# Kernel tuning notes

Hardware: AMD Instinct MI355X
Metric: run time of the kernel (lower is better)

## Reference

```python
import jax, jax.numpy as jnp
import numpy as np

E, TOPK, H, I = 8, 2, 2048, 5632
T = 4096


def setup_inputs() -> dict:
    key = jax.random.key(0)
    k1, k2, k3, k4 = jax.random.split(key, 4)
    hidden_states = jax.random.normal(k1, (T, H), dtype=jnp.float32)
    gate_w = jax.random.normal(k2, (E, H), dtype=jnp.float32) * (1.0 / np.sqrt(H))
    # fused gate+up projection: [E, 2*I, H]
    w13 = jax.random.normal(k3, (E, 2 * I, H), dtype=jnp.float32) * (1.0 / np.sqrt(H))
    # down projection: [E, H, I]
    w2 = jax.random.normal(k4, (E, H, I), dtype=jnp.float32) * (1.0 / np.sqrt(I))
    return {"hidden_states": hidden_states, "gate_w": gate_w, "w13": w13, "w2": w2, "top_k": TOPK}


def reference(hidden_states, gate_w, w13, w2, top_k):
    num_experts = gate_w.shape[0]
    inter = w2.shape[2]
    # router: fp32 gate logits -> softmax -> top-k -> renormalize (FusedMoE renormalize=True)
    logits = hidden_states.astype(jnp.float32) @ gate_w.T          # [T, E]
    probs = jax.nn.softmax(logits, axis=-1)
    vals, idx = jax.lax.top_k(probs, top_k)                        # [T, k]
    vals = vals / jnp.sum(vals, axis=-1, keepdims=True)
    # dense routing weight matrix [T, E] (zero outside top-k)
    dense_w = jnp.sum(jax.nn.one_hot(idx, num_experts, dtype=vals.dtype) * vals[..., None], axis=1)

    def body(acc, inputs):
        w13_e, w2_e, we = inputs                                   # [2I,H], [H,I], [T]
        gu = hidden_states @ w13_e.T                               # [T, 2I]
        g, u = gu[:, :inter], gu[:, inter:]
        h = jax.nn.silu(g) * u                                     # SwiGLU
        y = h @ w2_e.T                                             # [T, H]
        return acc + we[:, None] * y, None

    acc0 = jnp.zeros_like(hidden_states)
    out, _ = jax.lax.scan(body, acc0, (w13, w2, dense_w.T))
    return out
```

## Files before the change

### kernel.cpp

```cpp
#include <hip/hip_runtime.h>

#define T_TOK 4096
#define H_DIM 2048
#define I_DIM 5632
#define NE 8

typedef _Float16 f16;
typedef _Float16 f16x8 __attribute__((ext_vector_type(8)));
typedef _Float16 f16x4 __attribute__((ext_vector_type(4)));
typedef float f32x4 __attribute__((ext_vector_type(4)));

#define OFF_META   0
#define OFF_BTOK   256
#define OFF_BW     (256 + 32768)
#define OFF_RE     (256 + 2 * 32768)
#define OFF_RW     (256 + 3 * 32768)
#define OFF_HSB    (256 + 4 * 32768)
#define OFF_HB     (OFF_HSB + (size_t)T_TOK * H_DIM * 2)

__device__ __forceinline__ int swzk(int r, int bir) {
    return (bir & 15) | ((((bir >> 4) ^ r) & 7) << 4);
}

__device__ __forceinline__ f16x4 cvt4(float4 v) {
    f16x4 t; t[0] = (f16)v.x; t[1] = (f16)v.y; t[2] = (f16)v.z; t[3] = (f16)v.w; return t;
}

__global__ void cvt_hs_kernel(const float* __restrict__ hs, f16* __restrict__ hsb) {
    size_t i = ((size_t)blockIdx.x * 256 + threadIdx.x) * 8;
    float4 a = *(const float4*)(hs + i);
    float4 b = *(const float4*)(hs + i + 4);
    f16x8 v;
    v[0] = (f16)a.x; v[1] = (f16)a.y; v[2] = (f16)a.z; v[3] = (f16)a.w;
    v[4] = (f16)b.x; v[5] = (f16)b.y; v[6] = (f16)b.z; v[7] = (f16)b.w;
    *(f16x8*)(hsb + i) = v;
}

__global__ void gate_kernel(const float* __restrict__ hs, const float* __restrict__ gw,
                            int* __restrict__ re, float* __restrict__ rw,
                            int* __restrict__ counts) {
    int lane = threadIdx.x & 63;
    int t = blockIdx.x * 4 + (threadIdx.x >> 6);
    float acc[NE];
#pragma unroll
    for (int e = 0; e < NE; ++e) acc[e] = 0.f;
    const float* x = hs + (size_t)t * H_DIM;
    for (int i = lane; i < H_DIM; i += 64) {
        float xv = x[i];
#pragma unroll
        for (int e = 0; e < NE; ++e) acc[e] += xv * gw[e * H_DIM + i];
    }
#pragma unroll
    for (int e = 0; e < NE; ++e)
        for (int off = 32; off > 0; off >>= 1) acc[e] += __shfl_xor(acc[e], off);
    if (lane == 0) {
        int i1 = 0; float l1 = acc[0];
#pragma unroll
        for (int e = 1; e < NE; ++e) if (acc[e] > l1) { l1 = acc[e]; i1 = e; }
        int i2 = -1; float l2 = -1e30f;
#pragma unroll
        for (int e = 0; e < NE; ++e) if (e != i1 && acc[e] > l2) { l2 = acc[e]; i2 = e; }
        float aa = __expf(l2 - l1);
        float s = 1.f / (1.f + aa);
        re[t * 2] = i1; re[t * 2 + 1] = i2;
        rw[t * 2] = s;  rw[t * 2 + 1] = aa * s;
        atomicAdd(&counts[i1], 1);
        atomicAdd(&counts[i2], 1);
    }
}

__global__ void scan_kernel(int* __restrict__ meta) {
    if (threadIdx.x == 0) {
        int s = 0;
        for (int e = 0; e < NE; ++e) { meta[8 + e] = s; meta[16 + e] = s; s += meta[e]; }
    }
}

__global__ void place_kernel(const int* __restrict__ re, const float* __restrict__ rw,
                             int* __restrict__ cursor, int* __restrict__ btok,
                             float* __restrict__ bwv) {
    int t = blockIdx.x * 256 + threadIdx.x;
    if (t >= T_TOK) return;
#pragma unroll
    for (int s = 0; s < 2; ++s) {
        int e = re[t * 2 + s];
        int p = atomicAdd(&cursor[e], 1);
        btok[p] = t;
        bwv[p] = rw[t * 2 + s];
    }
}

__device__ __forceinline__ void decode_panel(int id, int npx, int e_arg,
                                             int& e, int& bx, int& by) {
    int sg  = id >> 8;
    int rem = id & 255;
    by = rem >> 3;
    int P = sg * 8 + (rem & 7);
    if (e_arg >= 0) { e = e_arg; bx = P; }
    else            { e = P / npx; bx = P % npx; }
}

__global__ __launch_bounds__(512) void gemm1_kernel(
    const float* __restrict__ w13, const f16* __restrict__ hsb, f16* __restrict__ hb,
    const int* __restrict__ counts, const int* __restrict__ offs,
    const int* __restrict__ btok, int e_arg, int global_h)
{
    int e, bx, by;
    decode_panel(blockIdx.x, 88, e_arg, e, bx, by);
    const int n_e = counts[e];
    if (by * 128 >= n_e) return;
    const int boff = offs[e];
    const float* We = w13 + (size_t)e * (2 * I_DIM) * H_DIM;

    const int tid = threadIdx.x;
    const int lane = tid & 63;
    const int wid = tid >> 6;
    const int wm = wid >> 1, wn = wid & 1;

    __shared__ f16 As0[128 * 64], As1[128 * 64];
    __shared__ f16 Bg0[64 * 64],  Bg1[64 * 64];
    __shared__ f16 Bu0[64 * 64],  Bu1[64 * 64];

    const f16* gA[2];
    int awadr[2];
#pragma unroll
    for (int i = 0; i < 2; ++i) {
        int c = i * 512 + tid;
        int r = c >> 3;
        int s = c & 7;
        int idx = by * 128 + r;
        idx = idx < n_e ? idx : n_e - 1;
        int tok = btok[boff + idx];
        gA[i] = hsb + (size_t)tok * H_DIM + s * 8;
        awadr[i] = r * 128 + swzk(r, s * 16);
    }
    const float* gBg[2]; const float* gBu[2];
    int bwadr[2];
#pragma unroll
    for (int j = 0; j < 2; ++j) {
        int c = j * 512 + tid;
        int r = c >> 4;
        int k4 = c & 15;
        gBg[j] = We + (size_t)(bx * 64 + r) * H_DIM + k4 * 4;
        gBu[j] = We + (size_t)(I_DIM + bx * 64 + r) * H_DIM + k4 * 4;
        bwadr[j] = r * 128 + swzk(r, k4 * 8);
    }

    f32x4 accg[2][2], accu[2][2];
#pragma unroll
    for (int m = 0; m < 2; ++m)
#pragma unroll
        for (int n = 0; n < 2; ++n) { accg[m][n] = (f32x4)0.f; accu[m][n] = (f32x4)0.f; }

    const int NT = H_DIM / 64;

    {
        f16x8 aP[2]; float4 gP[2], uP[2];
#pragma unroll
        for (int i = 0; i < 2; ++i) aP[i] = *(const f16x8*)(gA[i]);
#pragma unroll
        for (int j = 0; j < 2; ++j) { gP[j] = *(const float4*)gBg[j]; uP[j] = *(const float4*)gBu[j]; }
#pragma unroll
        for (int i = 0; i < 2; ++i) *(f16x8*)((char*)As0 + awadr[i]) = aP[i];
#pragma unroll
        for (int j = 0; j < 2; ++j) {
            *(f16x4*)((char*)Bg0 + bwadr[j]) = cvt4(gP[j]);
            *(f16x4*)((char*)Bu0 + bwadr[j]) = cvt4(uP[j]);
        }
        __syncthreads();
    }

#define G1_TILE(AsR, BgR, BuR, AsW, BgW, BuW, t)                                    \
    {                                                                               \
        const int kn = (((t) + 1 < NT) ? (t) + 1 : NT - 1) * 64;                    \
        f16x8 aN[2]; float4 gN[2], uN[2];                                           \
        _Pragma("unroll")                                                           \
        for (int i = 0; i < 2; ++i) aN[i] = *(const f16x8*)(gA[i] + kn);            \
        _Pragma("unroll")                                                           \
        for (int j = 0; j < 2; ++j) {                                               \
            gN[j] = *(const float4*)(gBg[j] + kn);                                  \
            uN[j] = *(const float4*)(gBu[j] + kn);                                  \
        }                                                                           \
        _Pragma("unroll")                                                           \
        for (int kh = 0; kh < 2; ++kh) {                                            \
            f16x8 a[2], bg[2], bu[2];                                               \
            const int kb = kh * 64 + (lane >> 4) * 16;                              \
            _Pragma("unroll")                                                       \
            for (int m = 0; m < 2; ++m) {                                           \
                int r = wm * 32 + m * 16 + (lane & 15);                             \
                a[m] = *(const f16x8*)((const char*)AsR + r * 128 + swzk(r, kb));   \
            }                                                                       \
            _Pragma("unroll")                                                       \
            for (int n = 0; n < 2; ++n) {                                           \
                int r = wn * 32 + n * 16 + (lane & 15);                             \
                bg[n] = *(const f16x8*)((const char*)BgR + r * 128 + swzk(r, kb));  \
                bu[n] = *(const f16x8*)((const char*)BuR + r * 128 + swzk(r, kb));  \
            }                                                                       \
            _Pragma("unroll")                                                       \
            for (int m = 0; m < 2; ++m)                                             \
                _Pragma("unroll")                                                   \
                for (int n = 0; n < 2; ++n) {                                       \
                    accg[m][n] = __builtin_amdgcn_mfma_f32_16x16x32_f16(a[m], bg[n], accg[m][n], 0, 0, 0); \
                    accu[m][n] = __builtin_amdgcn_mfma_f32_16x16x32_f16(a[m], bu[n], accu[m][n], 0, 0, 0); \
                }                                                                   \
        }                                                                           \
        _Pragma("unroll")                                                           \
        for (int i = 0; i < 2; ++i) *(f16x8*)((char*)AsW + awadr[i]) = aN[i];       \
        _Pragma("unroll")                                                           \
        for (int j = 0; j < 2; ++j) {                                               \
            *(f16x4*)((char*)BgW + bwadr[j]) = cvt4(gN[j]);                         \
            *(f16x4*)((char*)BuW + bwadr[j]) = cvt4(uN[j]);                         \
        }                                                                           \
        __syncthreads();                                                            \
    }

#pragma unroll 1
    for (int kt = 0; kt < NT; kt += 2) {
        G1_TILE(As0, Bg0, Bu0, As1, Bg1, Bu1, kt);
        G1_TILE(As1, Bg1, Bu1, As0, Bg0, Bu0, kt + 1);
    }
#undef G1_TILE

    const int hbase = (global_h ? boff : 0) + by * 128;
#pragma unroll
    for (int m = 0; m < 2; ++m) {
        int rl0 = wm * 32 + m * 16 + ((lane >> 4) << 2);
#pragma unroll
        for (int r = 0; r < 4; ++r) {
            int rl = rl0 + r;
            if (by * 128 + rl < n_e) {
#pragma unroll
                for (int n = 0; n < 2; ++n) {
                    float g = accg[m][n][r];
                    float u = accu[m][n][r];
                    float h = g / (1.f + __expf(-g)) * u;
                    hb[(size_t)(hbase + rl) * I_DIM + bx * 64 + wn * 32 + n * 16 + (lane & 15)] = (f16)h;
                }
            }
        }
    }
}

__global__ __launch_bounds__(512) void gemm2_kernel(
    const float* __restrict__ w2, const f16* __restrict__ hb, float* __restrict__ out,
    const int* __restrict__ counts, const int* __restrict__ offs,
    const int* __restrict__ btok, const float* __restrict__ bwv, int e_arg, int global_h)
{
    int e, bx, by;
    decode_panel(blockIdx.x, 16, e_arg, e, bx, by);
    const int n_e = counts[e];
    if (by * 128 >= n_e) return;
    const int boff = offs[e];
    const float* We = w2 + (size_t)e * H_DIM * I_DIM;

    const int tid = threadIdx.x;
    const int lane = tid & 63;
    const int wid = tid >> 6;
    const int wm = wid >> 1, wn = wid & 1;

    __shared__ f16 As0[128 * 64], As1[128 * 64];
    __shared__ f16 Bs0[128 * 64], Bs1[128 * 64];

    const int hbase = (global_h ? boff : 0) + by * 128;
    const f16* gA[2];
    int awadr[2];
#pragma unroll
    for (int i = 0; i < 2; ++i) {
        int c = i * 512 + tid;
        int r = c >> 3;
        int s = c & 7;
        gA[i] = hb + (size_t)(hbase + r) * I_DIM + s * 8;
        awadr[i] = r * 128 + swzk(r, s * 16);
    }
    const float* gB[4];
    int bwadr[4];
#pragma unroll
    for (int j = 0; j < 4; ++j) {
        int c = j * 512 + tid;
        int r = c >> 4;
        int k4 = c & 15;
        gB[j] = We + (size_t)(bx * 128 + r) * I_DIM + k4 * 4;
        bwadr[j] = r * 128 + swzk(r, k4 * 8);
    }

    f32x4 acc[2][4];
#pragma unroll
    for (int m = 0; m < 2; ++m)
#pragma unroll
        for (int n = 0; n < 4; ++n) acc[m][n] = (f32x4)0.f;

    const int NT = I_DIM / 64;

    {
        f16x8 aP[2]; float4 bP[4];
#pragma unroll
        for (int i = 0; i < 2; ++i) aP[i] = *(const f16x8*)(gA[i]);
#pragma unroll
        for (int j = 0; j < 4; ++j) bP[j] = *(const float4*)gB[j];
#pragma unroll
        for (int i = 0; i < 2; ++i) *(f16x8*)((char*)As0 + awadr[i]) = aP[i];
#pragma unroll
        for (int j = 0; j < 4; ++j) *(f16x4*)((char*)Bs0 + bwadr[j]) = cvt4(bP[j]);
        __syncthreads();
    }

#define G2_TILE(AsR, BsR, AsW, BsW, t)                                              \
    {                                                                               \
        const int kn = (((t) + 1 < NT) ? (t) + 1 : NT - 1) * 64;                    \
        f16x8 aN[2]; float4 bN[4];                                                  \
        _Pragma("unroll")                                                           \
        for (int i = 0; i < 2; ++i) aN[i] = *(const f16x8*)(gA[i] + kn);            \
        _Pragma("unroll")                                                           \
        for (int j = 0; j < 4; ++j) bN[j] = *(const float4*)(gB[j] + kn);           \
        _Pragma("unroll")                                                           \
        for (int kh = 0; kh < 2; ++kh) {                                            \
            f16x8 a[2], b[4];                                                       \
            const int kb = kh * 64 + (lane >> 4) * 16;                              \
            _Pragma("unroll")                                                       \
            for (int m = 0; m < 2; ++m) {                                           \
                int r = wm * 32 + m * 16 + (lane & 15);                             \
                a[m] = *(const f16x8*)((const char*)AsR + r * 128 + swzk(r, kb));   \
            }                                                                       \
            _Pragma("unroll")                                                       \
            for (int n = 0; n < 4; ++n) {                                           \
                int r = wn * 64 + n * 16 + (lane & 15);                             \
                b[n] = *(const f16x8*)((const char*)BsR + r * 128 + swzk(r, kb));   \
            }                                                                       \
            _Pragma("unroll")                                                       \
            for (int m = 0; m < 2; ++m)                                             \
                _Pragma("unroll")                                                   \
                for (int n = 0; n < 4; ++n)                                         \
                    acc[m][n] = __builtin_amdgcn_mfma_f32_16x16x32_f16(a[m], b[n], acc[m][n], 0, 0, 0); \
        }                                                                           \
        _Pragma("unroll")                                                           \
        for (int i = 0; i < 2; ++i) *(f16x8*)((char*)AsW + awadr[i]) = aN[i];       \
        _Pragma("unroll")                                                           \
        for (int j = 0; j < 4; ++j) *(f16x4*)((char*)BsW + bwadr[j]) = cvt4(bN[j]); \
        __syncthreads();                                                            \
    }

#pragma unroll 1
    for (int kt = 0; kt < NT; kt += 2) {
        G2_TILE(As0, Bs0, As1, Bs1, kt);
        G2_TILE(As1, Bs1, As0, Bs0, kt + 1);
    }
#undef G2_TILE

#pragma unroll
    for (int m = 0; m < 2; ++m) {
        int rl0 = wm * 32 + m * 16 + ((lane >> 4) << 2);
#pragma unroll
        for (int r = 0; r < 4; ++r) {
            int rl = rl0 + r;
            if (by * 128 + rl < n_e) {
                int p = boff + by * 128 + rl;
                int tok = btok[p];
                float w = bwv[p];
#pragma unroll
                for (int n = 0; n < 4; ++n)
                    atomicAdd(&out[(size_t)tok * H_DIM + bx * 128 + wn * 64 + n * 16 + (lane & 15)],
                              w * acc[m][n][r]);
            }
        }
    }
}

extern "C" void kernel_launch(void* const* d_in, const int* in_sizes, int n_in,
                              void* d_out, int out_size, void* d_ws, size_t ws_size,
                              hipStream_t stream) {
    const float* hs  = (const float*)d_in[0];
    const float* gw  = (const float*)d_in[1];
    const float* w13 = (const float*)d_in[2];
    const float* w2  = (const float*)d_in[3];
    float* out = (float*)d_out;

    char* ws = (char*)d_ws;
    int*   meta = (int*)(ws + OFF_META);
    int*   btok = (int*)(ws + OFF_BTOK);
    float* bwv  = (float*)(ws + OFF_BW);
    int*   re   = (int*)(ws + OFF_RE);
    float* rw   = (float*)(ws + OFF_RW);
    f16*   hsb  = (f16*)(ws + OFF_HSB);
    f16*   hb   = (f16*)(ws + OFF_HB);

    hipMemsetAsync(d_out, 0, (size_t)T_TOK * H_DIM * 4, stream);
    hipMemsetAsync(meta, 0, 256, stream);

    cvt_hs_kernel<<<(T_TOK * H_DIM) / (256 * 8), 256, 0, stream>>>(hs, hsb);
    gate_kernel<<<T_TOK / 4, 256, 0, stream>>>(hs, gw, re, rw, meta);
    scan_kernel<<<1, 64, 0, stream>>>(meta);
    place_kernel<<<T_TOK / 256, 256, 0, stream>>>(re, rw, meta + 16, btok, bwv);

    size_t need_allpairs = OFF_HB + (size_t)(2 * T_TOK + 128) * I_DIM * 2;
    if (ws_size >= need_allpairs) {
        gemm1_kernel<<<704 * 32, 512, 0, stream>>>(w13, hsb, hb, meta, meta + 8, btok, -1, 1);
        gemm2_kernel<<<128 * 32, 512, 0, stream>>>(w2, hb, out, meta, meta + 8, btok, bwv, -1, 1);
    } else {
        for (int e = 0; e < NE; ++e) {
            gemm1_kernel<<<88 * 32, 512, 0, stream>>>(w13, hsb, hb, meta, meta + 8, btok, e, 0);
            gemm2_kernel<<<16 * 32, 512, 0, stream>>>(w2, hb, out, meta, meta + 8, btok, bwv, e, 0);
        }
    }
}
```

Measured before the change: 1.330 ms.

## Pre-convert weights to fp16 and stream tiles via direct global-to-LDS loads

```diff
diff --git a/kernel.cpp b/kernel.cpp
--- a/kernel.cpp
+++ b/kernel.cpp
@@ -7,7 +7,6 @@
 
 typedef _Float16 f16;
 typedef _Float16 f16x8 __attribute__((ext_vector_type(8)));
-typedef _Float16 f16x4 __attribute__((ext_vector_type(4)));
 typedef float f32x4 __attribute__((ext_vector_type(4)));
 
 #define OFF_META   0
@@ -16,14 +15,26 @@
 #define OFF_RE     (256 + 2 * 32768)
 #define OFF_RW     (256 + 3 * 32768)
 #define OFF_HSB    (256 + 4 * 32768)
-#define OFF_HB     (OFF_HSB + (size_t)T_TOK * H_DIM * 2)
+#define OFF_WF     (OFF_HSB + (size_t)T_TOK * H_DIM * 2)
+
+typedef const __attribute__((address_space(1))) unsigned int guint;
+typedef __attribute__((address_space(3))) unsigned int luint;
 
 __device__ __forceinline__ int swzk(int r, int bir) {
     return (bir & 15) | ((((bir >> 4) ^ r) & 7) << 4);
 }
 
-__device__ __forceinline__ f16x4 cvt4(float4 v) {
-    f16x4 t; t[0] = (f16)v.x; t[1] = (f16)v.y; t[2] = (f16)v.z; t[3] = (f16)v.w; return t;
+__global__ void cvt_w_kernel(const float* __restrict__ src, f16* __restrict__ dst, int n8) {
+    int stride = gridDim.x * blockDim.x;
+    for (int i = blockIdx.x * blockDim.x + threadIdx.x; i < n8; i += stride) {
+        size_t b = (size_t)i * 8;
+        float4 a = *(const float4*)(src + b);
+        float4 c = *(const float4*)(src + b + 4);
+        f16x8 v;
+        v[0] = (f16)a.x; v[1] = (f16)a.y; v[2] = (f16)a.z; v[3] = (f16)a.w;
+        v[4] = (f16)c.x; v[5] = (f16)c.y; v[6] = (f16)c.z; v[7] = (f16)c.w;
+        *(f16x8*)(dst + b) = v;
+    }
 }
 
 __global__ void cvt_hs_kernel(const float* __restrict__ hs, f16* __restrict__ hsb) {
@@ -92,16 +103,16 @@
 
 __device__ __forceinline__ void decode_panel(int id, int npx, int e_arg,
                                              int& e, int& bx, int& by) {
+    if (e_arg >= 0) { e = e_arg; bx = id >> 5; by = id & 31; return; }
     int sg  = id >> 8;
     int rem = id & 255;
     by = rem >> 3;
     int P = sg * 8 + (rem & 7);
-    if (e_arg >= 0) { e = e_arg; bx = P; }
-    else            { e = P / npx; bx = P % npx; }
-}
-
-__global__ __launch_bounds__(512) void gemm1_kernel(
-    const float* __restrict__ w13, const f16* __restrict__ hsb, f16* __restrict__ hb,
+    e = P / npx; bx = P % npx;
+}
+
+__global__ __launch_bounds__(256, 2) void gemm1_kernel(
+    const f16* __restrict__ w13f, const f16* __restrict__ hsb, f16* __restrict__ hb,
     const int* __restrict__ counts, const int* __restrict__ offs,
     const int* __restrict__ btok, int e_arg, int global_h)
 {
@@ -110,139 +121,113 @@
     const int n_e = counts[e];
     if (by * 128 >= n_e) return;
     const int boff = offs[e];
-    const float* We = w13 + (size_t)e * (2 * I_DIM) * H_DIM;
+    const f16* We = (e_arg >= 0) ? w13f : (w13f + (size_t)e * (2 * I_DIM) * H_DIM);
 
     const int tid = threadIdx.x;
     const int lane = tid & 63;
     const int wid = tid >> 6;
     const int wm = wid >> 1, wn = wid & 1;
+    const int l15 = lane & 15;
 
     __shared__ f16 As0[128 * 64], As1[128 * 64];
-    __shared__ f16 Bg0[64 * 64],  Bg1[64 * 64];
-    __shared__ f16 Bu0[64 * 64],  Bu1[64 * 64];
-
-    const f16* gA[2];
-    int awadr[2];
-#pragma unroll
-    for (int i = 0; i < 2; ++i) {
-        int c = i * 512 + tid;
+    __shared__ f16 Bs0[128 * 64], Bs1[128 * 64];
+
+    const f16* gA[4]; const f16* gB[4]; int dstc[4];
+#pragma unroll
+    for (int i = 0; i < 4; ++i) {
+        int c = i * 256 + tid;
         int r = c >> 3;
-        int s = c & 7;
+        dstc[i] = c * 16;
+        int slot = ((c & 7) ^ (r & 7)) * 8;
         int idx = by * 128 + r;
         idx = idx < n_e ? idx : n_e - 1;
-        int tok = btok[boff + idx];
-        gA[i] = hsb + (size_t)tok * H_DIM + s * 8;
-        awadr[i] = r * 128 + swzk(r, s * 16);
-    }
-    const float* gBg[2]; const float* gBu[2];
-    int bwadr[2];
-#pragma unroll
-    for (int j = 0; j < 2; ++j) {
-        int c = j * 512 + tid;
-        int r = c >> 4;
-        int k4 = c & 15;
-        gBg[j] = We + (size_t)(bx * 64 + r) * H_DIM + k4 * 4;
-        gBu[j] = We + (size_t)(I_DIM + bx * 64 + r) * H_DIM + k4 * 4;
-        bwadr[j] = r * 128 + swzk(r, k4 * 8);
-    }
-
-    f32x4 accg[2][2], accu[2][2];
-#pragma unroll
-    for (int m = 0; m < 2; ++m)
-#pragma unroll
-        for (int n = 0; n < 2; ++n) { accg[m][n] = (f32x4)0.f; accu[m][n] = (f32x4)0.f; }
+        gA[i] = hsb + (size_t)btok[boff + idx] * H_DIM + slot;
+        int wrow = (r < 64) ? (bx * 64 + r) : (I_DIM + bx * 64 + (r - 64));
+        gB[i] = We + (size_t)wrow * H_DIM + slot;
+    }
+
+    f32x4 ag[4][2], au[4][2];
+#pragma unroll
+    for (int m = 0; m < 4; ++m)
+#pragma unroll
+        for (int n = 0; n < 2; ++n) { ag[m][n] = (f32x4)0.f; au[m][n] = (f32x4)0.f; }
 
     const int NT = H_DIM / 64;
 
-    {
-        f16x8 aP[2]; float4 gP[2], uP[2];
-#pragma unroll
-        for (int i = 0; i < 2; ++i) aP[i] = *(const f16x8*)(gA[i]);
-#pragma unroll
-        for (int j = 0; j < 2; ++j) { gP[j] = *(const float4*)gBg[j]; uP[j] = *(const float4*)gBu[j]; }
-#pragma unroll
-        for (int i = 0; i < 2; ++i) *(f16x8*)((char*)As0 + awadr[i]) = aP[i];
-#pragma unroll
-        for (int j = 0; j < 2; ++j) {
-            *(f16x4*)((char*)Bg0 + bwadr[j]) = cvt4(gP[j]);
-            *(f16x4*)((char*)Bu0 + bwadr[j]) = cvt4(uP[j]);
-        }
-        __syncthreads();
-    }
-
-#define G1_TILE(AsR, BgR, BuR, AsW, BgW, BuW, t)                                    \
+#pragma unroll
+    for (int i = 0; i < 4; ++i) {
+        __builtin_amdgcn_global_load_lds((guint*)gA[i], (luint*)((char*)As0 + dstc[i]), 16, 0, 0);
+        __builtin_amdgcn_global_load_lds((guint*)gB[i], (luint*)((char*)Bs0 + dstc[i]), 16, 0, 0);
+    }
+
+#define G1T(AR, BR, AW, BW, t)                                                      \
     {                                                                               \
-        const int kn = (((t) + 1 < NT) ? (t) + 1 : NT - 1) * 64;                    \
-        f16x8 aN[2]; float4 gN[2], uN[2];                                           \
-        _Pragma("unroll")                                                           \
-        for (int i = 0; i < 2; ++i) aN[i] = *(const f16x8*)(gA[i] + kn);            \
-        _Pragma("unroll")                                                           \
-        for (int j = 0; j < 2; ++j) {                                               \
-            gN[j] = *(const float4*)(gBg[j] + kn);                                  \
-            uN[j] = *(const float4*)(gBu[j] + kn);                                  \
+        __syncthreads();    \
+        if ((t) + 1 < NT) {                                                         \
+            const int k0 = ((t) + 1) * 64;                                          \
+            _Pragma("unroll")                                                       \
+            for (int i = 0; i < 4; ++i) {                                           \
+                __builtin_amdgcn_global_load_lds((guint*)(gA[i] + k0),              \
+                    (luint*)((char*)AW + dstc[i]), 16, 0, 0);                       \
+                __builtin_amdgcn_global_load_lds((guint*)(gB[i] + k0),              \
+                    (luint*)((char*)BW + dstc[i]), 16, 0, 0);                       \
+            }                                                                       \
         }                                                                           \
         _Pragma("unroll")                                                           \
         for (int kh = 0; kh < 2; ++kh) {                                            \
-            f16x8 a[2], bg[2], bu[2];                                               \
             const int kb = kh * 64 + (lane >> 4) * 16;                              \
-            _Pragma("unroll")                                                       \
-            for (int m = 0; m < 2; ++m) {                                           \
-                int r = wm * 32 + m * 16 + (lane & 15);                             \
-                a[m] = *(const f16x8*)((const char*)AsR + r * 128 + swzk(r, kb));   \
+            f16x8 a[4], bg[2], bu[2];                                               \
+            _Pragma("unroll")                                                       \
+            for (int m = 0; m < 4; ++m) {                                           \
+                int r = wm * 64 + m * 16 + l15;                                     \
+                a[m] = *(const f16x8*)((const char*)AR + r * 128 + swzk(r, kb));    \
             }                                                                       \
             _Pragma("unroll")                                                       \
             for (int n = 0; n < 2; ++n) {                                           \
-                int r = wn * 32 + n * 16 + (lane & 15);                             \
-                bg[n] = *(const f16x8*)((const char*)BgR + r * 128 + swzk(r, kb));  \
-                bu[n] = *(const f16x8*)((const char*)BuR + r * 128 + swzk(r, kb));  \
-            }                                                                       \
-            _Pragma("unroll")                                                       \
-            for (int m = 0; m < 2; ++m)                                             \
+                int rg = wn * 32 + n * 16 + l15;                                    \
+                bg[n] = *(const f16x8*)((const char*)BR + rg * 128 + swzk(rg, kb)); \
+                int ru = 64 + rg;                                                   \
+                bu[n] = *(const f16x8*)((const char*)BR + ru * 128 + swzk(ru, kb)); \
+            }                                                                       \
+            _Pragma("unroll")                                                       \
+            for (int m = 0; m < 4; ++m)                                             \
                 _Pragma("unroll")                                                   \
                 for (int n = 0; n < 2; ++n) {                                       \
-                    accg[m][n] = __builtin_amdgcn_mfma_f32_16x16x32_f16(a[m], bg[n], accg[m][n], 0, 0, 0); \
-                    accu[m][n] = __builtin_amdgcn_mfma_f32_16x16x32_f16(a[m], bu[n], accu[m][n], 0, 0, 0); \
+                    ag[m][n] = __builtin_amdgcn_mfma_f32_16x16x32_f16(a[m], bg[n], ag[m][n], 0, 0, 0); \
+                    au[m][n] = __builtin_amdgcn_mfma_f32_16x16x32_f16(a[m], bu[n], au[m][n], 0, 0, 0); \
                 }                                                                   \
         }                                                                           \
-        _Pragma("unroll")                                                           \
-        for (int i = 0; i < 2; ++i) *(f16x8*)((char*)AsW + awadr[i]) = aN[i];       \
-        _Pragma("unroll")                                                           \
-        for (int j = 0; j < 2; ++j) {                                               \
-            *(f16x4*)((char*)BgW + bwadr[j]) = cvt4(gN[j]);                         \
-            *(f16x4*)((char*)BuW + bwadr[j]) = cvt4(uN[j]);                         \
-        }                                                                           \
-        __syncthreads();                                                            \
     }
 
 #pragma unroll 1
     for (int kt = 0; kt < NT; kt += 2) {
-        G1_TILE(As0, Bg0, Bu0, As1, Bg1, Bu1, kt);
-        G1_TILE(As1, Bg1, Bu1, As0, Bg0, Bu0, kt + 1);
-    }
-#undef G1_TILE
+        G1T(As0, Bs0, As1, Bs1, kt);
+        G1T(As1, Bs1, As0, Bs0, kt + 1);
+    }
+#undef G1T
 
     const int hbase = (global_h ? boff : 0) + by * 128;
 #pragma unroll
-    for (int m = 0; m < 2; ++m) {
-        int rl0 = wm * 32 + m * 16 + ((lane >> 4) << 2);
+    for (int m = 0; m < 4; ++m) {
+        int rl0 = wm * 64 + m * 16 + ((lane >> 4) << 2);
 #pragma unroll
         for (int r = 0; r < 4; ++r) {
             int rl = rl0 + r;
             if (by * 128 + rl < n_e) {
 #pragma unroll
                 for (int n = 0; n < 2; ++n) {
-                    float g = accg[m][n][r];
-                    float u = accu[m][n][r];
+                    float g = ag[m][n][r];
+                    float u = au[m][n][r];
                     float h = g / (1.f + __expf(-g)) * u;
-                    hb[(size_t)(hbase + rl) * I_DIM + bx * 64 + wn * 32 + n * 16 + (lane & 15)] = (f16)h;
+                    hb[(size_t)(hbase + rl) * I_DIM + bx * 64 + wn * 32 + n * 16 + l15] = (f16)h;
                 }
             }
         }
     }
 }
 
-__global__ __launch_bounds__(512) void gemm2_kernel(
-    const float* __restrict__ w2, const f16* __restrict__ hb, float* __restrict__ out,
+__global__ __launch_bounds__(256, 2) void gemm2_kernel(
+    const f16* __restrict__ w2f, const f16* __restrict__ hb, float* __restrict__ out,
     const int* __restrict__ counts, const int* __restrict__ offs,
     const int* __restrict__ btok, const float* __restrict__ bwv, int e_arg, int global_h)
 {
@@ -251,104 +236,90 @@
     const int n_e = counts[e];
     if (by * 128 >= n_e) return;
     const int boff = offs[e];
-    const float* We = w2 + (size_t)e * H_DIM * I_DIM;
+    const f16* We = (e_arg >= 0) ? w2f : (w2f + (size_t)e * H_DIM * I_DIM);
 
     const int tid = threadIdx.x;
     const int lane = tid & 63;
     const int wid = tid >> 6;
     const int wm = wid >> 1, wn = wid & 1;
+    const int l15 = lane & 15;
 
     __shared__ f16 As0[128 * 64], As1[128 * 64];
     __shared__ f16 Bs0[128 * 64], Bs1[128 * 64];
 
-    const int hbase = (global_h ? boff : 0) + by * 128;
-    const f16* gA[2];
-    int awadr[2];
-#pragma unroll
-    for (int i = 0; i < 2; ++i) {
-        int c = i * 512 + tid;
+    const int hb0 = global_h ? boff : 0;
+    const f16* gA[4]; const f16* gB[4]; int dstc[4];
+#pragma unroll
+    for (int i = 0; i < 4; ++i) {
+        int c = i * 256 + tid;
         int r = c >> 3;
-        int s = c & 7;
-        gA[i] = hb + (size_t)(hbase + r) * I_DIM + s * 8;
-        awadr[i] = r * 128 + swzk(r, s * 16);
-    }
-    const float* gB[4];
-    int bwadr[4];
-#pragma unroll
-    for (int j = 0; j < 4; ++j) {
-        int c = j * 512 + tid;
-        int r = c >> 4;
-        int k4 = c & 15;
-        gB[j] = We + (size_t)(bx * 128 + r) * I_DIM + k4 * 4;
-        bwadr[j] = r * 128 + swzk(r, k4 * 8);
-    }
-
-    f32x4 acc[2][4];
-#pragma unroll
-    for (int m = 0; m < 2; ++m)
+        dstc[i] = c * 16;
+        int slot = ((c & 7) ^ (r & 7)) * 8;
+        int idx = by * 128 + r;
+        idx = idx < n_e ? idx : n_e - 1;
+        gA[i] = hb + (size_t)(hb0 + idx) * I_DIM + slot;
+        gB[i] = We + (size_t)(bx * 128 + r) * I_DIM + slot;
+    }
+
+    f32x4 acc[4][4];
+#pragma unroll
+    for (int m = 0; m < 4; ++m)
 #pragma unroll
         for (int n = 0; n < 4; ++n) acc[m][n] = (f32x4)0.f;
 
     const int NT = I_DIM / 64;
 
-    {
-        f16x8 aP[2]; float4 bP[4];
-#pragma unroll
-        for (int i = 0; i < 2; ++i) aP[i] = *(const f16x8*)(gA[i]);
-#pragma unroll
-        for (int j = 0; j < 4; ++j) bP[j] = *(const float4*)gB[j];
-#pragma unroll
-        for (int i = 0; i < 2; ++i) *(f16x8*)((char*)As0 + awadr[i]) = aP[i];
-#pragma unroll
-        for (int j = 0; j < 4; ++j) *(f16x4*)((char*)Bs0 + bwadr[j]) = cvt4(bP[j]);
-        __syncthreads();
-    }
-
-#define G2_TILE(AsR, BsR, AsW, BsW, t)                                              \
+#pragma unroll
+    for (int i = 0; i < 4; ++i) {
+        __builtin_amdgcn_global_load_lds((guint*)gA[i], (luint*)((char*)As0 + dstc[i]), 16, 0, 0);
+        __builtin_amdgcn_global_load_lds((guint*)gB[i], (luint*)((char*)Bs0 + dstc[i]), 16, 0, 0);
+    }
+
+#define G2T(AR, BR, AW, BW, t)                                                      \
     {                                                                               \
-        const int kn = (((t) + 1 < NT) ? (t) + 1 : NT - 1) * 64;                    \
-        f16x8 aN[2]; float4 bN[4];                                                  \
-        _Pragma("unroll")                                                           \
-        for (int i = 0; i < 2; ++i) aN[i] = *(const f16x8*)(gA[i] + kn);            \
-        _Pragma("unroll")                                                           \
-        for (int j = 0; j < 4; ++j) bN[j] = *(const float4*)(gB[j] + kn);           \
+        __syncthreads();                                                            \
+        if ((t) + 1 < NT) {                                                         \
+            const int k0 = ((t) + 1) * 64;                                          \
+            _Pragma("unroll")                                                       \
+            for (int i = 0; i < 4; ++i) {                                           \
+                __builtin_amdgcn_global_load_lds((guint*)(gA[i] + k0),              \
+                    (luint*)((char*)AW + dstc[i]), 16, 0, 0);                       \
+                __builtin_amdgcn_global_load_lds((guint*)(gB[i] + k0),              \
+                    (luint*)((char*)BW + dstc[i]), 16, 0, 0);                       \
+            }                                                                       \
+        }                                                                           \
         _Pragma("unroll")                                                           \
         for (int kh = 0; kh < 2; ++kh) {                                            \
-            f16x8 a[2], b[4];                                                       \
             const int kb = kh * 64 + (lane >> 4) * 16;                              \
-            _Pragma("unroll")                                                       \
-            for (int m = 0; m < 2; ++m) {                                           \
-                int r = wm * 32 + m * 16 + (lane & 15);                             \
-                a[m] = *(const f16x8*)((const char*)AsR + r * 128 + swzk(r, kb));   \
+            f16x8 a[4], b[4];                                                       \
+            _Pragma("unroll")                                                       \
+            for (int m = 0; m < 4; ++m) {                                           \
+                int r = wm * 64 + m * 16 + l15;                                     \
+                a[m] = *(const f16x8*)((const char*)AR + r * 128 + swzk(r, kb));    \
             }                                                                       \
             _Pragma("unroll")                                                       \
             for (int n = 0; n < 4; ++n) {                                           \
-                int r = wn * 64 + n * 16 + (lane & 15);                             \
-                b[n] = *(const f16x8*)((const char*)BsR + r * 128 + swzk(r, kb));   \
-            }                                                                       \
-            _Pragma("unroll")                                                       \
-            for (int m = 0; m < 2; ++m)                                             \
+                int r = wn * 64 + n * 16 + l15;                                     \
+                b[n] = *(const f16x8*)((const char*)BR + r * 128 + swzk(r, kb));    \
+            }                                                                       \
+            _Pragma("unroll")                                                       \
+            for (int m = 0; m < 4; ++m)                                             \
                 _Pragma("unroll")                                                   \
                 for (int n = 0; n < 4; ++n)                                         \
                     acc[m][n] = __builtin_amdgcn_mfma_f32_16x16x32_f16(a[m], b[n], acc[m][n], 0, 0, 0); \
         }                                                                           \
-        _Pragma("unroll")                                                           \
-        for (int i = 0; i < 2; ++i) *(f16x8*)((char*)AsW + awadr[i]) = aN[i];       \
-        _Pragma("unroll")                                                           \
-        for (int j = 0; j < 4; ++j) *(f16x4*)((char*)BsW + bwadr[j]) = cvt4(bN[j]); \
-        __syncthreads();                                                            \
     }
 
 #pragma unroll 1
     for (int kt = 0; kt < NT; kt += 2) {
-        G2_TILE(As0, Bs0, As1, Bs1, kt);
-        G2_TILE(As1, Bs1, As0, Bs0, kt + 1);
-    }
-#undef G2_TILE
-
-#pragma unroll
-    for (int m = 0; m < 2; ++m) {
-        int rl0 = wm * 32 + m * 16 + ((lane >> 4) << 2);
+        G2T(As0, Bs0, As1, Bs1, kt);
+        G2T(As1, Bs1, As0, Bs0, kt + 1);
+    }
+#undef G2T
+
+#pragma unroll
+    for (int m = 0; m < 4; ++m) {
+        int rl0 = wm * 64 + m * 16 + ((lane >> 4) << 2);
 #pragma unroll
         for (int r = 0; r < 4; ++r) {
             int rl = rl0 + r;
@@ -358,7 +329,7 @@
                 float w = bwv[p];
 #pragma unroll
                 for (int n = 0; n < 4; ++n)
-                    atomicAdd(&out[(size_t)tok * H_DIM + bx * 128 + wn * 64 + n * 16 + (lane & 15)],
+                    atomicAdd(&out[(size_t)tok * H_DIM + bx * 128 + wn * 64 + n * 16 + l15],
                               w * acc[m][n][r]);
             }
         }
@@ -381,7 +352,6 @@
     int*   re   = (int*)(ws + OFF_RE);
     float* rw   = (float*)(ws + OFF_RW);
     f16*   hsb  = (f16*)(ws + OFF_HSB);
-    f16*   hb   = (f16*)(ws + OFF_HB);
 
     hipMemsetAsync(d_out, 0, (size_t)T_TOK * H_DIM * 4, stream);
     hipMemsetAsync(meta, 0, 256, stream);
@@ -391,14 +361,39 @@
     scan_kernel<<<1, 64, 0, stream>>>(meta);
     place_kernel<<<T_TOK / 256, 256, 0, stream>>>(re, rw, meta + 16, btok, bwv);
 
-    size_t need_allpairs = OFF_HB + (size_t)(2 * T_TOK + 128) * I_DIM * 2;
-    if (ws_size >= need_allpairs) {
-        gemm1_kernel<<<704 * 32, 512, 0, stream>>>(w13, hsb, hb, meta, meta + 8, btok, -1, 1);
-        gemm2_kernel<<<128 * 32, 512, 0, stream>>>(w2, hb, out, meta, meta + 8, btok, bwv, -1, 1);
+    const size_t w13_elems = (size_t)NE * 2 * I_DIM * H_DIM;
+    const size_t w2_elems  = (size_t)NE * H_DIM * I_DIM;
+
+    size_t o_w13f = OFF_WF;
+    size_t o_w2f  = o_w13f + w13_elems * 2;
+    size_t o_hb   = o_w2f + w2_elems * 2;
+    size_t need_full = o_hb + (size_t)2 * T_TOK * I_DIM * 2;
+
+    size_t f_w13 = OFF_WF;
+    size_t f_w2  = f_w13 + (size_t)2 * I_DIM * H_DIM * 2;
+    size_t f_hb  = f_w2 + (size_t)H_DIM * I_DIM * 2;
+    size_t need_pe = f_hb + (size_t)T_TOK * I_DIM * 2;
+    (void)need_pe;
+
+    if (ws_size >= need_full) {
+        f16* w13f = (f16*)(ws + o_w13f);
+        f16* w2f  = (f16*)(ws + o_w2f);
+        f16* hb   = (f16*)(ws + o_hb);
+        cvt_w_kernel<<<2048, 256, 0, stream>>>(w13, w13f, (int)(w13_elems / 8));
+        cvt_w_kernel<<<2048, 256, 0, stream>>>(w2,  w2f,  (int)(w2_elems / 8));
+        gemm1_kernel<<<704 * 32, 256, 0, stream>>>(w13f, hsb, hb, meta, meta + 8, btok, -1, 1);
+        gemm2_kernel<<<128 * 32, 256, 0, stream>>>(w2f, hb, out, meta, meta + 8, btok, bwv, -1, 1);
     } else {
+        f16* w13f = (f16*)(ws + f_w13);
+        f16* w2f  = (f16*)(ws + f_w2);
+        f16* hb   = (f16*)(ws + f_hb);
         for (int e = 0; e < NE; ++e) {
-            gemm1_kernel<<<88 * 32, 512, 0, stream>>>(w13, hsb, hb, meta, meta + 8, btok, e, 0);
-            gemm2_kernel<<<16 * 32, 512, 0, stream>>>(w2, hb, out, meta, meta + 8, btok, bwv, e, 0);
+            cvt_w_kernel<<<1024, 256, 0, stream>>>(w13 + (size_t)e * 2 * I_DIM * H_DIM, w13f,
+                                                   (int)((size_t)2 * I_DIM * H_DIM / 8));
+            gemm1_kernel<<<88 * 32, 256, 0, stream>>>(w13f, hsb, hb, meta, meta + 8, btok, e, 0);
+            cvt_w_kernel<<<1024, 256, 0, stream>>>(w2 + (size_t)e * H_DIM * I_DIM, w2f,
+                                                   (int)((size_t)H_DIM * I_DIM / 8));
+            gemm2_kernel<<<16 * 32, 256, 0, stream>>>(w2f, hb, out, meta, meta + 8, btok, bwv, e, 0);
         }
     }
 }
```

New measurement: 1.278 ms. 1.04x faster.
